# Performance work log

Hardware: AMD Instinct MI355X
Metric: run time of the kernel (lower is better)

The kernel has to match this reference:

```python
import jax, jax.numpy as jnp
import numpy as np

WH, WW = 8, 8
N = WH * WW
H = 12
DIM = 384
HD = DIM // H
NW = 36
B_ = 2304


def _coords_table_norm8_log():
    # SwinV2-style log-spaced continuous relative coords, 'norm8_log'
    rh = np.arange(-(WH - 1), WH, dtype=np.float32)
    rw = np.arange(-(WW - 1), WW, dtype=np.float32)
    t = np.stack(np.meshgrid(rh, rw, indexing='ij'), axis=-1)[None]  # (1,15,15,2)
    t[..., 0] /= (WH - 1)
    t[..., 1] /= (WW - 1)
    t *= 8
    t = np.sign(t) * np.log2(np.abs(t) + 1.0) / np.log2(8)
    return jnp.asarray(t, dtype=jnp.float32)


def _relative_position_index():
    ch, cw = np.meshgrid(np.arange(WH), np.arange(WW), indexing='ij')
    cf = np.stack([ch.reshape(-1), cw.reshape(-1)])  # (2, N)
    rel = cf[:, :, None] - cf[:, None, :]            # (2, N, N)
    rel = rel.transpose(1, 2, 0).astype(np.int32)
    rel[..., 0] += WH - 1
    rel[..., 1] += WW - 1
    rel[..., 0] *= 2 * WW - 1
    return jnp.asarray(rel.sum(-1), dtype=jnp.int32)  # (N, N)


def setup_inputs() -> dict:
    key = jax.random.key(0)
    ks = jax.random.split(key, 10)
    std = 0.02
    x = jax.random.normal(ks[0], (B_, N, DIM), dtype=jnp.float32)
    # shifted-window style 0 / -100 mask
    m = jax.random.uniform(ks[1], (NW, N, N))
    mask = jnp.where(m < 0.25, jnp.float32(-100.0), jnp.float32(0.0))
    qkv_w = jax.random.normal(ks[2], (3 * DIM, DIM), dtype=jnp.float32) * std
    q_bias = jnp.zeros((DIM,), dtype=jnp.float32)
    v_bias = jnp.zeros((DIM,), dtype=jnp.float32)
    rpe_w1 = jax.random.normal(ks[3], (512, 2), dtype=jnp.float32) * std
    rpe_b1 = jnp.zeros((512,), dtype=jnp.float32)
    rpe_w2 = jax.random.normal(ks[4], (H, 512), dtype=jnp.float32) * std
    proj_w = jax.random.normal(ks[5], (DIM, DIM), dtype=jnp.float32) * std
    proj_b = jnp.zeros((DIM,), dtype=jnp.float32)
    return {
        'x': x, 'mask': mask, 'qkv_w': qkv_w, 'q_bias': q_bias, 'v_bias': v_bias,
        'rpe_w1': rpe_w1, 'rpe_b1': rpe_b1, 'rpe_w2': rpe_w2,
        'proj_w': proj_w, 'proj_b': proj_b,
        'coords_table': _coords_table_norm8_log(),
        'rel_index': _relative_position_index(),
    }


def reference(x, mask, qkv_w, q_bias, v_bias, rpe_w1, rpe_b1, rpe_w2,
              proj_w, proj_b, coords_table, rel_index):
    B, n, C = x.shape
    scale = jnp.float32(HD) ** -0.5
    # qkv with k-bias removed (q_bias, zeros, v_bias)
    qkv_b = jnp.concatenate([q_bias, jnp.zeros_like(v_bias), v_bias])
    qkv = x @ qkv_w.T + qkv_b                                   # (B, N, 3C)
    qkv = qkv.reshape(B, n, 3, H, HD).transpose(2, 0, 3, 1, 4)   # (3, B, H, N, hd)
    q, k, v = qkv[0], qkv[1], qkv[2]
    # fp32 attention logits
    attn = jnp.einsum('bhnd,bhmd->bhnm', (q * scale).astype(jnp.float32),
                      k.astype(jnp.float32))                     # (B, H, N, N)
    # MLP-based relative position bias: (1,15,15,2) -> (225, H)
    hmid = jax.nn.relu(coords_table @ rpe_w1.T + rpe_b1)
    table = (hmid @ rpe_w2.T).reshape(-1, H)                     # (225, H)
    bias = table[rel_index.reshape(-1)].reshape(n, n, H)
    bias = bias.transpose(2, 0, 1)                               # (H, N, N)
    attn = attn + bias[None]
    # shift mask: (nW, N, N) broadcast over batch groups and heads
    nW = mask.shape[0]
    attn = attn.reshape(B // nW, nW, H, n, n) + mask[None, :, None]
    attn = attn.reshape(B, H, n, n)
    attn = jax.nn.softmax(attn, axis=-1).astype(x.dtype)
    out = jnp.einsum('bhnm,bhmd->bhnd', attn, v)
    out = out.transpose(0, 2, 1, 3).reshape(B, n, C)
    return out @ proj_w.T + proj_b
```

## Files before the change

### kernel.cpp

```cpp
#include <hip/hip_runtime.h>

typedef __attribute__((ext_vector_type(8))) __bf16 bf16x8;
typedef __attribute__((ext_vector_type(4))) float f4;
typedef __attribute__((ext_vector_type(2))) unsigned int u32x2;

#define MFMA(a, b, c) __builtin_amdgcn_mfma_f32_16x16x32_bf16((a), (b), (c), 0, 0, 0)


__device__ inline unsigned pk2(float a, float b) {
  unsigned short ha = __builtin_bit_cast(unsigned short, (__bf16)a);
  unsigned short hb = __builtin_bit_cast(unsigned short, (__bf16)b);
  return (unsigned)ha | ((unsigned)hb << 16);
}

__global__ void k_rpe_table(const float* __restrict__ coords,
                            const float* __restrict__ w1,
                            const float* __restrict__ b1,
                            const float* __restrict__ w2,
                            float* __restrict__ table) {
  const int p = blockIdx.x;
  const int lane = threadIdx.x;
  const float c0 = coords[p * 2 + 0], c1 = coords[p * 2 + 1];
  float hm[8];
#pragma unroll
  for (int t = 0; t < 8; ++t) {
    const int j = lane * 8 + t;
    float v = fmaf(c0, w1[j * 2 + 0], fmaf(c1, w1[j * 2 + 1], b1[j]));
    hm[t] = v > 0.f ? v : 0.f;
  }
  for (int h = 0; h < 12; ++h) {
    float s = 0.f;
#pragma unroll
    for (int t = 0; t < 8; ++t) s = fmaf(hm[t], w2[h * 512 + lane * 8 + t], s);
    for (int off = 32; off >= 1; off >>= 1) s += __shfl_xor(s, off);
    if (lane == 0) table[p * 12 + h] = s;
  }
}

__global__ void k_bias_gather(const float* __restrict__ table,
                              const int* __restrict__ rel,
                              float* __restrict__ bias_t) {
  const int idx = blockIdx.x * 256 + threadIdx.x;
  const int h = idx >> 12;
  const int r = idx & 4095;
  bias_t[idx] = table[rel[r] * 12 + h];
}

__global__ void k_maskbits(const float* __restrict__ mask,
                           unsigned long long* __restrict__ maskb) {
  const int i = blockIdx.x * 64 + threadIdx.x;
  const float* mrow = mask + (size_t)i * 64;
  unsigned long long bits = 0ull;
#pragma unroll
  for (int k = 0; k < 64; ++k)
    bits |= (unsigned long long)(mrow[k] < -50.f ? 1u : 0u) << k;
  maskb[i] = bits;
}

__global__ void k_pack_w(const float* __restrict__ qkv_w,
                         const float* __restrict__ proj_w,
                         __bf16* __restrict__ qkvp,
                         __bf16* __restrict__ projp) {
  const int gid = blockIdx.x * 256 + threadIdx.x;
  const int frag = gid >> 6, lane = gid & 63;
  const int lr = lane & 15, lhi = lane >> 4;
  const float* src;
  __bf16* dst;
  if (frag < 864) {
    const int nb = frag / 12, ks = frag % 12;
    src = qkv_w + (nb * 16 + lr) * 384 + ks * 32 + lhi * 8;
    dst = qkvp + (size_t)frag * 512 + lane * 8;
  } else {
    const int f2 = frag - 864;
    const int nb = f2 / 12, ks = f2 % 12;
    src = proj_w + (nb * 16 + lr) * 384 + ks * 32 + lhi * 8;
    dst = projp + (size_t)f2 * 512 + lane * 8;
  }
#pragma unroll
  for (int j = 0; j < 8; ++j) dst[j] = (__bf16)src[j];
}

__global__ __launch_bounds__(768, 3) void k_fused(
    const float* __restrict__ x, const unsigned long long* __restrict__ maskb,
    const float* __restrict__ q_bias, const float* __restrict__ v_bias,
    const float* __restrict__ bias_t, const bf16x8* __restrict__ qkvp,
    const bf16x8* __restrict__ projp, const float* __restrict__ proj_b,
    float* __restrict__ out) {
  __shared__ __align__(16) char lds[159744];
  const int tid = threadIdx.x;
  const int b = blockIdx.x;
  const int w = tid >> 6, lane = tid & 63;
  const int lr = lane & 15, lhi = lane >> 4;
  const int h = w;
  char* wb = lds + 49152 + w * 9216;
  const int mb = b % 36;
  const float scale = 0.17677669529663687f;
  const f4 fz = {0.f, 0.f, 0.f, 0.f};

  const bf16x8* fq = qkvp + h * 1536 + lane;
  const bf16x8* fk = qkvp + 18432 + h * 1536 + lane;
  const bf16x8* fv = qkvp + 36864 + h * 1536 + lane;
  bf16x8 cq0 = fq[0], cq1 = fq[768];
  bf16x8 ck0 = fk[0], ck1 = fk[768];
  bf16x8 cv0 = fv[0], cv1 = fv[768];

  {
    const f4* xp = (const f4*)(x + (size_t)b * 24576);
#pragma unroll
    for (int it = 0; it < 8; ++it) {
      const int idx = tid + it * 768;
      const int row = idx / 96;
      const int c4 = idx % 96;
      f4 v = xp[idx];
      unsigned long long pkw =
          (unsigned long long)pk2(v[0], v[1]) |
          ((unsigned long long)pk2(v[2], v[3]) << 32);
      *(unsigned long long*)(lds + row * 768 + ((c4 * 8) ^ ((row & 7) << 4))) = pkw;
    }
  }
  __syncthreads();

  unsigned pkv[4][2][2];
  {
    f4 aq[4][2], ak[4][2], av[4][2];
#pragma unroll
    for (int mi = 0; mi < 4; ++mi)
#pragma unroll
      for (int nj = 0; nj < 2; ++nj) {
        aq[mi][nj] = fz;
        ak[mi][nj] = fz;
        av[mi][nj] = fz;
      }
#pragma unroll
    for (int ks = 0; ks < 12; ++ks) {
#pragma unroll
      for (int mi = 0; mi < 4; ++mi) {
        const int row = mi * 16 + lr;
        const bf16x8 a = *(const bf16x8*)(lds + row * 768 +
                                          ((ks * 64 + lhi * 16) ^ ((row & 7) << 4)));
        __builtin_amdgcn_s_setprio(1);
        aq[mi][0] = MFMA(a, cq0, aq[mi][0]);
        aq[mi][1] = MFMA(a, cq1, aq[mi][1]);
        ak[mi][0] = MFMA(a, ck0, ak[mi][0]);
        ak[mi][1] = MFMA(a, ck1, ak[mi][1]);
        av[mi][0] = MFMA(a, cv0, av[mi][0]);
        av[mi][1] = MFMA(a, cv1, av[mi][1]);
        __builtin_amdgcn_s_setprio(0);
      }
      const int kn = ks < 11 ? ks + 1 : 0;
      cq0 = fq[kn * 64];
      cq1 = fq[(12 + kn) * 64];
      ck0 = fk[kn * 64];
      ck1 = fk[(12 + kn) * 64];
      cv0 = fv[kn * 64];
      cv1 = fv[(12 + kn) * 64];
    }
    const float qb0 = q_bias[h * 32 + lr], qb1 = q_bias[h * 32 + 16 + lr];
    const float vb0 = v_bias[h * 32 + lr], vb1 = v_bias[h * 32 + 16 + lr];
#pragma unroll
    for (int mi = 0; mi < 4; ++mi) {
#pragma unroll
      for (int r = 0; r < 4; ++r) {
        const int row = mi * 16 + lhi * 4 + r;
        *(__bf16*)(wb + row * 72 + lr * 2) = (__bf16)((aq[mi][0][r] + qb0) * scale);
        *(__bf16*)(wb + row * 72 + (16 + lr) * 2) = (__bf16)((aq[mi][1][r] + qb1) * scale);
        *(__bf16*)(wb + 4608 + row * 72 + lr * 2) = (__bf16)ak[mi][0][r];
        *(__bf16*)(wb + 4608 + row * 72 + (16 + lr) * 2) = (__bf16)ak[mi][1][r];
      }
      pkv[mi][0][0] = pk2(av[mi][0][0] + vb0, av[mi][0][1] + vb0);
      pkv[mi][0][1] = pk2(av[mi][0][2] + vb0, av[mi][0][3] + vb0);
      pkv[mi][1][0] = pk2(av[mi][1][0] + vb1, av[mi][1][1] + vb1);
      pkv[mi][1][1] = pk2(av[mi][1][2] + vb1, av[mi][1][3] + vb1);
    }
  }

  f4 st[4][4];
  {
    bf16x8 fqv[4], fkv[4];
#pragma unroll
    for (int i = 0; i < 4; ++i) {
      const int rt = i * 16 + lr;
      fqv[i] = *(const bf16x8*)(wb + rt * 72 + lhi * 16);
      fkv[i] = *(const bf16x8*)(wb + 4608 + rt * 72 + lhi * 16);
    }
    __builtin_amdgcn_s_setprio(1);
#pragma unroll
    for (int mi = 0; mi < 4; ++mi)
#pragma unroll
      for (int nj = 0; nj < 4; ++nj) st[mi][nj] = MFMA(fkv[mi], fqv[nj], fz);
    __builtin_amdgcn_s_setprio(0);
  }

  {
    const float* bp = bias_t + h * 4096;
    const unsigned long long* mbp = maskb + mb * 64;
#pragma unroll
    for (int nj = 0; nj < 4; ++nj) {
      const int q = nj * 16 + lr;
      const unsigned long long mbits = mbp[q];
      float lsum = 0.f;
#pragma unroll
      for (int mi = 0; mi < 4; ++mi) {
        const int kbase = mi * 16 + lhi * 4;
        const f4 bb = *(const f4*)(bp + q * 64 + kbase);
        const unsigned b4 = (unsigned)(mbits >> kbase) & 0xFu;
        f4 e;
#pragma unroll
        for (int r = 0; r < 4; ++r)
          e[r] = ((b4 >> r) & 1u) ? 0.f : __expf(st[mi][nj][r] + bb[r]);
        st[mi][nj] = e;
        lsum += (e[0] + e[1]) + (e[2] + e[3]);
      }
      lsum += __shfl_xor(lsum, 16);
      lsum += __shfl_xor(lsum, 32);
      const float inv = 1.0f / lsum;
#pragma unroll
      for (int mi = 0; mi < 4; ++mi) {
        u32x2 pw;
        pw[0] = pk2(st[mi][nj][0] * inv, st[mi][nj][1] * inv);
        pw[1] = pk2(st[mi][nj][2] * inv, st[mi][nj][3] * inv);
        *(u32x2*)(wb + q * 144 + mi * 32 + lhi * 8) = pw;
      }
    }
  }

  f4 o[4][2];
#pragma unroll
  for (int mi = 0; mi < 4; ++mi) {
    o[mi][0] = fz;
    o[mi][1] = fz;
  }
  {
    const int srcA = lr + 32 * (lhi & 1);
    const int srcB = srcA + 16;
    const bool hiSel = lhi >= 2;
#pragma unroll
    for (int kh = 0; kh < 2; ++kh) {
      bf16x8 pa[4];
#pragma unroll
      for (int mi = 0; mi < 4; ++mi) {
        const int row = mi * 16 + lr;
        pa[mi] = *(const bf16x8*)(wb + row * 144 + kh * 64 + lhi * 16);
      }
      bf16x8 vv[2];
#pragma unroll
      for (int nj = 0; nj < 2; ++nj) {
        const unsigned a0 = (unsigned)__shfl((int)pkv[2 * kh][nj][0], srcA);
        const unsigned b0 = (unsigned)__shfl((int)pkv[2 * kh + 1][nj][0], srcA);
        const unsigned a1 = (unsigned)__shfl((int)pkv[2 * kh][nj][1], srcA);
        const unsigned b1 = (unsigned)__shfl((int)pkv[2 * kh + 1][nj][1], srcA);
        const unsigned a2 = (unsigned)__shfl((int)pkv[2 * kh][nj][0], srcB);
        const unsigned b2 = (unsigned)__shfl((int)pkv[2 * kh + 1][nj][0], srcB);
        const unsigned a3 = (unsigned)__shfl((int)pkv[2 * kh][nj][1], srcB);
        const unsigned b3 = (unsigned)__shfl((int)pkv[2 * kh + 1][nj][1], srcB);
        union {
          unsigned u[4];
          bf16x8 v8;
        } cv;
        cv.u[0] = hiSel ? b0 : a0;
        cv.u[1] = hiSel ? b1 : a1;
        cv.u[2] = hiSel ? b2 : a2;
        cv.u[3] = hiSel ? b3 : a3;
        vv[nj] = cv.v8;
      }
      __builtin_amdgcn_s_setprio(1);
#pragma unroll
      for (int mi = 0; mi < 4; ++mi) {
        o[mi][0] = MFMA(pa[mi], vv[0], o[mi][0]);
        o[mi][1] = MFMA(pa[mi], vv[1], o[mi][1]);
      }
      __builtin_amdgcn_s_setprio(0);
    }
  }

  const bf16x8* fw = projp + w * 1536 + lane;
  bf16x8 cw0 = fw[0], cw1 = fw[768];

#pragma unroll
  for (int mi = 0; mi < 4; ++mi) {
#pragma unroll
    for (int r = 0; r < 4; ++r) {
      const int row = mi * 16 + lhi * 4 + r;
      *(__bf16*)(wb + row * 72 + lr * 2) = (__bf16)o[mi][0][r];
      *(__bf16*)(wb + row * 72 + (16 + lr) * 2) = (__bf16)o[mi][1][r];
    }
  }
  __syncthreads();

  {
    f4 po[4][2];
#pragma unroll
    for (int mi = 0; mi < 4; ++mi) {
      po[mi][0] = fz;
      po[mi][1] = fz;
    }
    bf16x8 a[4];
#pragma unroll
    for (int mi = 0; mi < 4; ++mi) {
      const int row = mi * 16 + lr;
      a[mi] = *(const bf16x8*)(lds + 49152 + row * 72 + lhi * 16);
    }
#pragma unroll
    for (int ks = 0; ks < 12; ++ks) {
      const int kn = ks < 11 ? ks + 1 : 0;
      bf16x8 an[4];
#pragma unroll
      for (int mi = 0; mi < 4; ++mi) {
        const int row = mi * 16 + lr;
        an[mi] = *(const bf16x8*)(lds + 49152 + kn * 9216 + row * 72 + lhi * 16);
      }
      const bf16x8 nw0 = fw[kn * 64], nw1 = fw[(12 + kn) * 64];
      __builtin_amdgcn_s_setprio(1);
#pragma unroll
      for (int mi = 0; mi < 4; ++mi) {
        po[mi][0] = MFMA(a[mi], cw0, po[mi][0]);
        po[mi][1] = MFMA(a[mi], cw1, po[mi][1]);
      }
      __builtin_amdgcn_s_setprio(0);
#pragma unroll
      for (int mi = 0; mi < 4; ++mi) a[mi] = an[mi];
      cw0 = nw0; cw1 = nw1;
    }
    float* ob = out + (size_t)b * 24576;
    const float pb0 = proj_b[w * 32 + lr];
    const float pb1 = proj_b[w * 32 + 16 + lr];
#pragma unroll
    for (int mi = 0; mi < 4; ++mi) {
#pragma unroll
      for (int r = 0; r < 4; ++r) {
        const int row = mi * 16 + lhi * 4 + r;
        ob[row * 384 + w * 32 + lr] = po[mi][0][r] + pb0;
        ob[row * 384 + w * 32 + 16 + lr] = po[mi][1][r] + pb1;
      }
    }
  }
}

extern "C" void kernel_launch(void* const* d_in, const int* in_sizes, int n_in,
                              void* d_out, int out_size, void* d_ws, size_t ws_size,
                              hipStream_t stream) {
  const float* x = (const float*)d_in[0];
  const float* mask = (const float*)d_in[1];
  const float* qkv_w = (const float*)d_in[2];
  const float* q_bias = (const float*)d_in[3];
  const float* v_bias = (const float*)d_in[4];
  const float* rpe_w1 = (const float*)d_in[5];
  const float* rpe_b1 = (const float*)d_in[6];
  const float* rpe_w2 = (const float*)d_in[7];
  const float* proj_w = (const float*)d_in[8];
  const float* proj_b = (const float*)d_in[9];
  const float* coords = (const float*)d_in[10];
  const int* rel = (const int*)d_in[11];
  float* out = (float*)d_out;

  char* ws = (char*)d_ws;
  float* bias_t = (float*)(ws);
  __bf16* qkvp = (__bf16*)(ws + 196608);
  __bf16* projp = (__bf16*)(ws + 1081344);
  float* table = (float*)(ws + 1376256);
  unsigned long long* maskb = (unsigned long long*)(ws + 1387056);

  k_rpe_table<<<225, 64, 0, stream>>>(coords, rpe_w1, rpe_b1, rpe_w2, table);
  k_bias_gather<<<192, 256, 0, stream>>>(table, rel, bias_t);
  k_maskbits<<<36, 64, 0, stream>>>(mask, maskb);
  k_pack_w<<<288, 256, 0, stream>>>(qkv_w, proj_w, qkvp, projp);
  k_fused<<<2304, 768, 0, stream>>>(x, maskb, q_bias, v_bias, bias_t,
                                    (const bf16x8*)qkvp, (const bf16x8*)projp,
                                    proj_b, out);
}
```

Baseline: 317.7 us.

## Merge prep kernels, batch LDS loads before MFMAs, prefetch mask and bias

Three small prep kernels (weight packing, mask bit packing, RPE table MLP) are folded into one launch with block-range dispatch, which removes two kernel launches and their gaps. In the fused kernel's QKV GEMM, all four A fragments are loaded from LDS before the MFMA burst, and the priority toggle wraps the whole burst instead of each row tile. The mask bits and the first bias vector are fetched before the QK^T MFMAs so their global-load latency overlaps with compute. The cost is more live registers under a 768-thread launch bound.

```diff
diff --git a/kernel.cpp b/kernel.cpp
--- a/kernel.cpp
+++ b/kernel.cpp
@@ -13,27 +13,62 @@
   return (unsigned)ha | ((unsigned)hb << 16);
 }
 
-__global__ void k_rpe_table(const float* __restrict__ coords,
-                            const float* __restrict__ w1,
-                            const float* __restrict__ b1,
-                            const float* __restrict__ w2,
-                            float* __restrict__ table) {
-  const int p = blockIdx.x;
-  const int lane = threadIdx.x;
-  const float c0 = coords[p * 2 + 0], c1 = coords[p * 2 + 1];
-  float hm[8];
-#pragma unroll
-  for (int t = 0; t < 8; ++t) {
-    const int j = lane * 8 + t;
-    float v = fmaf(c0, w1[j * 2 + 0], fmaf(c1, w1[j * 2 + 1], b1[j]));
-    hm[t] = v > 0.f ? v : 0.f;
-  }
-  for (int h = 0; h < 12; ++h) {
-    float s = 0.f;
-#pragma unroll
-    for (int t = 0; t < 8; ++t) s = fmaf(hm[t], w2[h * 512 + lane * 8 + t], s);
-    for (int off = 32; off >= 1; off >>= 1) s += __shfl_xor(s, off);
-    if (lane == 0) table[p * 12 + h] = s;
+__global__ void k_prep(const float* __restrict__ qkv_w,
+                       const float* __restrict__ proj_w,
+                       const float* __restrict__ mask,
+                       const float* __restrict__ coords,
+                       const float* __restrict__ w1,
+                       const float* __restrict__ b1,
+                       const float* __restrict__ w2,
+                       __bf16* __restrict__ qkvp, __bf16* __restrict__ projp,
+                       unsigned long long* __restrict__ maskb,
+                       float* __restrict__ table) {
+  const int blk = blockIdx.x;
+  if (blk < 288) {
+    const int gid = blk * 256 + threadIdx.x;
+    const int frag = gid >> 6, lane = gid & 63;
+    const int lr = lane & 15, lhi = lane >> 4;
+    const float* src;
+    __bf16* dst;
+    if (frag < 864) {
+      const int nb = frag / 12, ks = frag % 12;
+      src = qkv_w + (nb * 16 + lr) * 384 + ks * 32 + lhi * 8;
+      dst = qkvp + (size_t)frag * 512 + lane * 8;
+    } else {
+      const int f2 = frag - 864;
+      const int nb = f2 / 12, ks = f2 % 12;
+      src = proj_w + (nb * 16 + lr) * 384 + ks * 32 + lhi * 8;
+      dst = projp + (size_t)f2 * 512 + lane * 8;
+    }
+#pragma unroll
+    for (int j = 0; j < 8; ++j) dst[j] = (__bf16)src[j];
+  } else if (blk < 297) {
+    const int i = (blk - 288) * 256 + threadIdx.x;
+    const float* mrow = mask + (size_t)i * 64;
+    unsigned long long bits = 0ull;
+#pragma unroll
+    for (int k = 0; k < 64; ++k)
+      bits |= (unsigned long long)(mrow[k] < -50.f ? 1u : 0u) << k;
+    maskb[i] = bits;
+  } else {
+    const int p = (blk - 297) * 4 + (threadIdx.x >> 6);
+    const int lane = threadIdx.x & 63;
+    if (p >= 225) return;
+    const float c0 = coords[p * 2 + 0], c1 = coords[p * 2 + 1];
+    float hm[8];
+#pragma unroll
+    for (int t = 0; t < 8; ++t) {
+      const int j = lane * 8 + t;
+      float v = fmaf(c0, w1[j * 2 + 0], fmaf(c1, w1[j * 2 + 1], b1[j]));
+      hm[t] = v > 0.f ? v : 0.f;
+    }
+    for (int h = 0; h < 12; ++h) {
+      float s = 0.f;
+#pragma unroll
+      for (int t = 0; t < 8; ++t) s = fmaf(hm[t], w2[h * 512 + lane * 8 + t], s);
+      for (int off = 32; off >= 1; off >>= 1) s += __shfl_xor(s, off);
+      if (lane == 0) table[p * 12 + h] = s;
+    }
   }
 }
 
@@ -44,40 +79,6 @@
   const int h = idx >> 12;
   const int r = idx & 4095;
   bias_t[idx] = table[rel[r] * 12 + h];
-}
-
-__global__ void k_maskbits(const float* __restrict__ mask,
-                           unsigned long long* __restrict__ maskb) {
-  const int i = blockIdx.x * 64 + threadIdx.x;
-  const float* mrow = mask + (size_t)i * 64;
-  unsigned long long bits = 0ull;
-#pragma unroll
-  for (int k = 0; k < 64; ++k)
-    bits |= (unsigned long long)(mrow[k] < -50.f ? 1u : 0u) << k;
-  maskb[i] = bits;
-}
-
-__global__ void k_pack_w(const float* __restrict__ qkv_w,
-                         const float* __restrict__ proj_w,
-                         __bf16* __restrict__ qkvp,
-                         __bf16* __restrict__ projp) {
-  const int gid = blockIdx.x * 256 + threadIdx.x;
-  const int frag = gid >> 6, lane = gid & 63;
-  const int lr = lane & 15, lhi = lane >> 4;
-  const float* src;
-  __bf16* dst;
-  if (frag < 864) {
-    const int nb = frag / 12, ks = frag % 12;
-    src = qkv_w + (nb * 16 + lr) * 384 + ks * 32 + lhi * 8;
-    dst = qkvp + (size_t)frag * 512 + lane * 8;
-  } else {
-    const int f2 = frag - 864;
-    const int nb = f2 / 12, ks = f2 % 12;
-    src = proj_w + (nb * 16 + lr) * 384 + ks * 32 + lhi * 8;
-    dst = projp + (size_t)f2 * 512 + lane * 8;
-  }
-#pragma unroll
-  for (int j = 0; j < 8; ++j) dst[j] = (__bf16)src[j];
 }
 
 __global__ __launch_bounds__(768, 3) void k_fused(
@@ -133,20 +134,24 @@
       }
 #pragma unroll
     for (int ks = 0; ks < 12; ++ks) {
+      bf16x8 a[4];
 #pragma unroll
       for (int mi = 0; mi < 4; ++mi) {
         const int row = mi * 16 + lr;
-        const bf16x8 a = *(const bf16x8*)(lds + row * 768 +
-                                          ((ks * 64 + lhi * 16) ^ ((row & 7) << 4)));
-        __builtin_amdgcn_s_setprio(1);
-        aq[mi][0] = MFMA(a, cq0, aq[mi][0]);
-        aq[mi][1] = MFMA(a, cq1, aq[mi][1]);
-        ak[mi][0] = MFMA(a, ck0, ak[mi][0]);
-        ak[mi][1] = MFMA(a, ck1, ak[mi][1]);
-        av[mi][0] = MFMA(a, cv0, av[mi][0]);
-        av[mi][1] = MFMA(a, cv1, av[mi][1]);
-        __builtin_amdgcn_s_setprio(0);
-      }
+        a[mi] = *(const bf16x8*)(lds + row * 768 +
+                                 ((ks * 64 + lhi * 16) ^ ((row & 7) << 4)));
+      }
+      __builtin_amdgcn_s_setprio(1);
+#pragma unroll
+      for (int mi = 0; mi < 4; ++mi) {
+        aq[mi][0] = MFMA(a[mi], cq0, aq[mi][0]);
+        aq[mi][1] = MFMA(a[mi], cq1, aq[mi][1]);
+        ak[mi][0] = MFMA(a[mi], ck0, ak[mi][0]);
+        ak[mi][1] = MFMA(a[mi], ck1, ak[mi][1]);
+        av[mi][0] = MFMA(a[mi], cv0, av[mi][0]);
+        av[mi][1] = MFMA(a[mi], cv1, av[mi][1]);
+      }
+      __builtin_amdgcn_s_setprio(0);
       const int kn = ks < 11 ? ks + 1 : 0;
       cq0 = fq[kn * 64];
       cq1 = fq[(12 + kn) * 64];
@@ -174,6 +179,17 @@
     }
   }
 
+  const float* bp = bias_t + h * 4096;
+  const unsigned long long* mbp = maskb + mb * 64;
+  unsigned long long mbits[4];
+  f4 bb0[4];
+#pragma unroll
+  for (int nj = 0; nj < 4; ++nj) {
+    const int q = nj * 16 + lr;
+    mbits[nj] = mbp[q];
+    bb0[nj] = *(const f4*)(bp + q * 64 + lhi * 4);
+  }
+
   f4 st[4][4];
   {
     bf16x8 fqv[4], fkv[4];
@@ -192,18 +208,15 @@
   }
 
   {
-    const float* bp = bias_t + h * 4096;
-    const unsigned long long* mbp = maskb + mb * 64;
 #pragma unroll
     for (int nj = 0; nj < 4; ++nj) {
       const int q = nj * 16 + lr;
-      const unsigned long long mbits = mbp[q];
       float lsum = 0.f;
 #pragma unroll
       for (int mi = 0; mi < 4; ++mi) {
         const int kbase = mi * 16 + lhi * 4;
-        const f4 bb = *(const f4*)(bp + q * 64 + kbase);
-        const unsigned b4 = (unsigned)(mbits >> kbase) & 0xFu;
+        const f4 bb = (mi == 0) ? bb0[nj] : *(const f4*)(bp + q * 64 + kbase);
+        const unsigned b4 = (unsigned)(mbits[nj] >> kbase) & 0xFu;
         f4 e;
 #pragma unroll
         for (int r = 0; r < 4; ++r)
@@ -319,7 +332,8 @@
       __builtin_amdgcn_s_setprio(0);
 #pragma unroll
       for (int mi = 0; mi < 4; ++mi) a[mi] = an[mi];
-      cw0 = nw0; cw1 = nw1;
+      cw0 = nw0;
+      cw1 = nw1;
     }
     float* ob = out + (size_t)b * 24576;
     const float pb0 = proj_b[w * 32 + lr];
@@ -360,10 +374,9 @@
   float* table = (float*)(ws + 1376256);
   unsigned long long* maskb = (unsigned long long*)(ws + 1387056);
 
-  k_rpe_table<<<225, 64, 0, stream>>>(coords, rpe_w1, rpe_b1, rpe_w2, table);
+  k_prep<<<354, 256, 0, stream>>>(qkv_w, proj_w, mask, coords, rpe_w1, rpe_b1,
+                                  rpe_w2, qkvp, projp, maskb, table);
   k_bias_gather<<<192, 256, 0, stream>>>(table, rel, bias_t);
-  k_maskbits<<<36, 64, 0, stream>>>(mask, maskb);
-  k_pack_w<<<288, 256, 0, stream>>>(qkv_w, proj_w, qkvp, projp);
   k_fused<<<2304, 768, 0, stream>>>(x, maskb, q_bias, v_bias, bias_t,
                                     (const bf16x8*)qkvp, (const bf16x8*)projp,
                                     proj_b, out);
```

Result: slower. 342.1 us (+7.7%).
